# Performance work log

Hardware: AMD Instinct MI355X
Metric: run time of the kernel (lower is better)

Reference implementation:

```python
import jax, jax.numpy as jnp
import numpy as np

EPS = 1e-5  # torch LayerNorm default

def layernorm(x, gamma, beta):
    mu = jnp.mean(x, axis=-1, keepdims=True)
    var = jnp.mean(jnp.square(x - mu), axis=-1, keepdims=True)
    return (x - mu) * jax.lax.rsqrt(var + EPS) * gamma + beta

def setup_inputs() -> dict:
    key = jax.random.key(0)
    ks = jax.random.split(key, 8)
    B, S, D = 4, 2048, 1024
    s = 1.0 / np.sqrt(D)  # torch Linear init scale
    return {
        "x": jax.random.normal(ks[0], (B, S, D), dtype=jnp.float32),
        "Wq": jax.random.uniform(ks[1], (D, D), jnp.float32, -s, s),
        "bq": jax.random.uniform(ks[2], (D,), jnp.float32, -s, s),
        "Wk": jax.random.uniform(ks[3], (D, D), jnp.float32, -s, s),
        "bk": jax.random.uniform(ks[4], (D,), jnp.float32, -s, s),
        "Wv": jax.random.uniform(ks[5], (D, D), jnp.float32, -s, s),
        "bv": jax.random.uniform(ks[6], (D,), jnp.float32, -s, s),
        "gamma": jnp.ones((D,), jnp.float32),
        "beta": jnp.zeros((D,), jnp.float32),
    }

def reference(x, Wq, bq, Wk, bk, Wv, bv, gamma, beta):
    # torch Linear: x @ W.T + b; shared LayerNorm applied to each projection
    q = layernorm(jnp.einsum('bsd,ed->bse', x, Wq) + bq, gamma, beta)
    k = layernorm(jnp.einsum('bsd,ed->bse', x, Wk) + bk, gamma, beta)
    v = layernorm(jnp.einsum('bsd,ed->bse', x, Wv) + bv, gamma, beta)
    att = jnp.einsum('bqd,bkd->bqk', q, k)  # no 1/sqrt(d) scaling in original
    att = jax.nn.softmax(att, axis=-1)
    # dropout is identity in eval mode (reference baseline)
    return jnp.einsum('bqk,bkd->bqd', att, v)
```

## Files before the change

kernel.cpp:

```cpp
#include <hip/hip_runtime.h>

typedef _Float16 f16;
typedef __attribute__((ext_vector_type(4))) _Float16 f16x4;
typedef __attribute__((ext_vector_type(8))) _Float16 f16x8;
typedef __attribute__((ext_vector_type(4))) float f32x4;

#define GLB_AS __attribute__((address_space(1)))
#define LDS_AS __attribute__((address_space(3)))

__device__ __forceinline__ void async_copy16(const void* g, void* l) {
  __builtin_amdgcn_global_load_lds((const GLB_AS void*)g, (LDS_AS void*)l, 16, 0, 0);
}

#define WAITVM(N) asm volatile("s_waitcnt vmcnt(" #N ")" ::: "memory")
#define WAITLGKM0() asm volatile("s_waitcnt lgkmcnt(0)" ::: "memory")
#define BAR() __builtin_amdgcn_s_barrier()
#define SB0() __builtin_amdgcn_sched_barrier(0)

#define STAGE_A(t_, kk_) do {                                                \
    const long _k = (long)(t_) * 64 + (kk_) * 32;                            \
    f16* _d = &Ash[(t_) & 1][kk_][w16 * 32];                                 \
    async_copy16(Ag + _k, _d);                                               \
    if constexpr (IA == 2) async_copy16(Ag + _k + 128l * lda, _d + 4096);    \
  } while (0)
#define STAGE_B(t_, kk_) do {                                                \
    const long _k = (long)(t_) * 64 + (kk_) * 32;                            \
    f16* _d = &Bsh[(t_) & 1][kk_][w16 * 32];                                 \
    async_copy16(Bg + _k, _d);                                               \
    async_copy16(Bg + _k + 128l * ldb, _d + 4096);                           \
  } while (0)

template <int BM, int BN, typename OutT, int MODE, bool BIAS>
__global__ __launch_bounds__(512, 2) void gemm8p(
    const f16* __restrict__ A, const f16* __restrict__ B, OutT* __restrict__ C,
    int lda, int ldb, int ldc, int K, long sA, long sB, long sC,
    int tiles_x, int tiles_y,
    const float* __restrict__ b0, const float* __restrict__ b1,
    const float* __restrict__ b2)
{
  constexpr int WM = BM / 2, WN = BN / 4;
  constexpr int RM = WM / 16, RN = WN / 16;
  constexpr int IA = BM / 128;
  static_assert(RN == 4 && BN == 256, "template assumes BN=256");

  __shared__ __align__(16) f16 Ash[2][2][BM * 32];
  __shared__ __align__(16) f16 Bsh[2][2][BN * 32];

  int bx, by, bz;
  {
    const int n = blockIdx.x;
    if (MODE == 0) {
      by = n % tiles_y;
      const int r = n / tiles_y;
      bx = r % tiles_x;
      bz = r / tiles_x;
    } else {
      const int j = n & 7, i = n >> 3, th = tiles_y >> 1;
      bz = j >> 1;
      bx = i / th;
      by = (j & 1) * th + i % th;
    }
  }

  A += (long)bz * sA;
  B += (long)bz * sB;
  C += (long)bz * sC;

  const int tid  = threadIdx.x;
  const int wave = tid >> 6, lane = tid & 63;
  const int wr = wave >> 2, wc = wave & 3;
  const int m0 = by * BM, n0 = bx * BN;
  const int r16 = lane & 15, quad = lane >> 4;
  const int w16 = wave * 16;

  const int cg8 = (((lane & 3) ^ ((lane >> 2) & 3) ^ ((lane >> 4) & 3)) * 8);
  const f16* Ag = A + (long)(m0 + w16 + (lane >> 2)) * lda + cg8;
  const f16* Bg = B + (long)(n0 + w16 + (lane >> 2)) * ldb + cg8;

  const int NT = K / 64;

  STAGE_A(0, 0); STAGE_B(0, 0);
  STAGE_A(0, 1); STAGE_B(0, 1);
  STAGE_A(1, 0); STAGE_B(1, 0);

  f32x4 acc[RM][RN] = {};

  const int rc  = (quad ^ ((r16 ^ (r16 >> 2)) & 3)) * 8;
  const int rdA = (wr * WM + r16) * 32 + rc;
  const int rdB = (wc * WN + r16) * 32 + rc;

  if constexpr (RM == 8) { WAITVM(8); } else { WAITVM(6); }
  BAR();

  for (int t = 0; t < NT; ++t) {
    const int bp = t & 1;
    const f16* A0 = &Ash[bp][0][0];
    const f16* A1 = &Ash[bp][1][0];
    const f16* B0 = &Bsh[bp][0][0];
    const f16* B1 = &Bsh[bp][1][0];
    f16x8 af[4], bf[4];

    if constexpr (RM == 4) {
#pragma unroll
      for (int i = 0; i < 4; i++) af[i] = *(const f16x8*)&A0[rdA + i * 512];
#pragma unroll
      for (int j = 0; j < 4; j++) bf[j] = *(const f16x8*)&B0[rdB + j * 512];
      if (t + 1 < NT) { STAGE_A(t + 1, 1); STAGE_B(t + 1, 1); }
      BAR();
      WAITLGKM0(); SB0();
      __builtin_amdgcn_s_setprio(1);
#pragma unroll
      for (int i = 0; i < 4; i++)
#pragma unroll
        for (int j = 0; j < 4; j++)
          acc[i][j] = __builtin_amdgcn_mfma_f32_16x16x32_f16(af[i], bf[j], acc[i][j], 0, 0, 0);
      __builtin_amdgcn_s_setprio(0); SB0();
      if (t < NT - 1) { WAITVM(6); } else { WAITVM(0); }
      BAR();
#pragma unroll
      for (int i = 0; i < 4; i++) af[i] = *(const f16x8*)&A1[rdA + i * 512];
#pragma unroll
      for (int j = 0; j < 4; j++) bf[j] = *(const f16x8*)&B1[rdB + j * 512];
      if (t + 2 < NT) { STAGE_A(t + 2, 0); STAGE_B(t + 2, 0); }
      BAR();
      WAITLGKM0(); SB0();
      __builtin_amdgcn_s_setprio(1);
#pragma unroll
      for (int i = 0; i < 4; i++)
#pragma unroll
        for (int j = 0; j < 4; j++)
          acc[i][j] = __builtin_amdgcn_mfma_f32_16x16x32_f16(af[i], bf[j], acc[i][j], 0, 0, 0);
      __builtin_amdgcn_s_setprio(0); SB0();
      if (t < NT - 2) { WAITVM(6); } else if (t == NT - 2) { WAITVM(3); } else { WAITVM(0); }
      BAR();
    } else {
#pragma unroll
      for (int i = 0; i < 4; i++) af[i] = *(const f16x8*)&A0[rdA + i * 512];
#pragma unroll
      for (int j = 0; j < 4; j++) bf[j] = *(const f16x8*)&B0[rdB + j * 512];
      if (t + 1 < NT) STAGE_A(t + 1, 1);
      BAR();
      WAITLGKM0(); SB0();
      __builtin_amdgcn_s_setprio(1);
#pragma unroll
      for (int i = 0; i < 4; i++)
#pragma unroll
        for (int j = 0; j < 4; j++)
          acc[i][j] = __builtin_amdgcn_mfma_f32_16x16x32_f16(af[i], bf[j], acc[i][j], 0, 0, 0);
      __builtin_amdgcn_s_setprio(0); SB0();
      BAR();
#pragma unroll
      for (int i = 0; i < 4; i++) af[i] = *(const f16x8*)&A0[rdA + (4 + i) * 512];
      if (t + 1 < NT) STAGE_B(t + 1, 1);
      BAR();
      WAITLGKM0(); SB0();
      __builtin_amdgcn_s_setprio(1);
#pragma unroll
      for (int i = 0; i < 4; i++)
#pragma unroll
        for (int j = 0; j < 4; j++)
          acc[4 + i][j] = __builtin_amdgcn_mfma_f32_16x16x32_f16(af[i], bf[j], acc[4 + i][j], 0, 0, 0);
      __builtin_amdgcn_s_setprio(0); SB0();
      if (t < NT - 1) { WAITVM(6); } else { WAITVM(0); }
      BAR();
#pragma unroll
      for (int i = 0; i < 4; i++) af[i] = *(const f16x8*)&A1[rdA + i * 512];
#pragma unroll
      for (int j = 0; j < 4; j++) bf[j] = *(const f16x8*)&B1[rdB + j * 512];
      if (t + 2 < NT) STAGE_A(t + 2, 0);
      BAR();
      WAITLGKM0(); SB0();
      __builtin_amdgcn_s_setprio(1);
#pragma unroll
      for (int i = 0; i < 4; i++)
#pragma unroll
        for (int j = 0; j < 4; j++)
          acc[i][j] = __builtin_amdgcn_mfma_f32_16x16x32_f16(af[i], bf[j], acc[i][j], 0, 0, 0);
      __builtin_amdgcn_s_setprio(0); SB0();
      BAR();
#pragma unroll
      for (int i = 0; i < 4; i++) af[i] = *(const f16x8*)&A1[rdA + (4 + i) * 512];
      if (t + 2 < NT) STAGE_B(t + 2, 0);
      BAR();
      WAITLGKM0(); SB0();
      __builtin_amdgcn_s_setprio(1);
#pragma unroll
      for (int i = 0; i < 4; i++)
#pragma unroll
        for (int j = 0; j < 4; j++)
          acc[4 + i][j] = __builtin_amdgcn_mfma_f32_16x16x32_f16(af[i], bf[j], acc[4 + i][j], 0, 0, 0);
      __builtin_amdgcn_s_setprio(0); SB0();
      if (t < NT - 2) { WAITVM(6); } else if (t == NT - 2) { WAITVM(4); } else { WAITVM(0); }
      BAR();
    }
  }

  float bias_j[RN];
#pragma unroll
  for (int j = 0; j < RN; j++) bias_j[j] = 0.f;
  if constexpr (BIAS) {
    const float* bias = (bz == 0) ? b0 : (bz == 1) ? b1 : b2;
#pragma unroll
    for (int j = 0; j < RN; j++) bias_j[j] = bias[n0 + wc * WN + j * 16 + r16];
  }
#pragma unroll
  for (int i = 0; i < RM; i++)
#pragma unroll
    for (int j = 0; j < RN; j++)
#pragma unroll
      for (int r = 0; r < 4; r++) {
        long row = m0 + wr * WM + i * 16 + quad * 4 + r;
        long col = n0 + wc * WN + j * 16 + r16;
        C[row * (long)ldc + col] = (OutT)(acc[i][j][r] + bias_j[j]);
      }
}

__global__ __launch_bounds__(256) void cast_all(
    const float* __restrict__ x, const float* __restrict__ Wq,
    const float* __restrict__ Wk, const float* __restrict__ Wv,
    f16* __restrict__ Xh, f16* __restrict__ Wh)
{
  const long off = (long)blockIdx.x * 1024 + threadIdx.x * 4;
  const float* src;
  f16* dst;
  if (off < 8388608L) {
    src = x + off;
    dst = Xh + off;
  } else {
    const long o = off - 8388608L;
    src = (o < 1048576L) ? Wq + o
        : (o < 2097152L) ? Wk + (o - 1048576L)
                         : Wv + (o - 2097152L);
    dst = Wh + o;
  }
  const float4 v = *(const float4*)src;
  f16x4 h;
  h.x = (f16)v.x; h.y = (f16)v.y; h.z = (f16)v.z; h.w = (f16)v.w;
  *(f16x4*)dst = h;
}

__global__ __launch_bounds__(256) void ln_kernel(
    f16* __restrict__ P, const float* __restrict__ gamma,
    const float* __restrict__ beta)
{
  f16* p = P + (long)blockIdx.y * 8388608 + (long)blockIdx.x * 1024;
  const int tid = threadIdx.x;
  const int e = tid * 4;

  f16x4 raw = *(const f16x4*)(p + e);
  float v0 = (float)raw.x, v1 = (float)raw.y;
  float v2 = (float)raw.z, v3 = (float)raw.w;
  float s  = v0 + v1 + v2 + v3;
  float s2 = v0 * v0 + v1 * v1 + v2 * v2 + v3 * v3;

#pragma unroll
  for (int off = 32; off > 0; off >>= 1) {
    s  += __shfl_down(s, off, 64);
    s2 += __shfl_down(s2, off, 64);
  }
  __shared__ float red[10];
  const int wave = tid >> 6, lane = tid & 63;
  if (lane == 0) { red[wave] = s; red[4 + wave] = s2; }
  __syncthreads();
  if (tid == 0) {
    red[8] = red[0] + red[1] + red[2] + red[3];
    red[9] = red[4] + red[5] + red[6] + red[7];
  }
  __syncthreads();
  const float mu   = red[8] * (1.f / 1024.f);
  const float var  = red[9] * (1.f / 1024.f) - mu * mu;
  const float rstd = rsqrtf(var + 1e-5f);

  float4 gg = *(const float4*)(gamma + e);
  float4 be = *(const float4*)(beta + e);
  f16x4 o;
  o.x = (f16)((v0 - mu) * rstd * gg.x + be.x);
  o.y = (f16)((v1 - mu) * rstd * gg.y + be.y);
  o.z = (f16)((v2 - mu) * rstd * gg.z + be.z);
  o.w = (f16)((v3 - mu) * rstd * gg.w + be.w);
  *(f16x4*)(p + e) = o;
}

__global__ __launch_bounds__(256) void transpose_kernel(const f16* __restrict__ V,
                                                        f16* __restrict__ Vt)
{
  const int S = 2048, D = 1024;
  const f16* v = V + (long)blockIdx.z * ((long)S * D);
  f16* vt = Vt + (long)blockIdx.z * ((long)D * S);
  __shared__ f16 tile[64][66];
  const int d0 = blockIdx.x * 64, j0 = blockIdx.y * 64;
  const int tx = threadIdx.x & 63, ty = threadIdx.x >> 6;
#pragma unroll
  for (int r = ty; r < 64; r += 4)
    tile[r][tx] = v[(long)(j0 + r) * D + d0 + tx];
  __syncthreads();
#pragma unroll
  for (int r = ty; r < 64; r += 4)
    vt[(long)(d0 + r) * S + j0 + tx] = tile[tx][r];
}

__global__ __launch_bounds__(256) void softmax_kernel(float* __restrict__ Sc)
{
  float* srow = Sc + (long)blockIdx.x * 2048;
  const int tid = threadIdx.x;
  float4 a = ((const float4*)srow)[tid];
  float4 b = ((const float4*)srow)[256 + tid];

  float m = fmaxf(fmaxf(fmaxf(a.x, a.y), fmaxf(a.z, a.w)),
                  fmaxf(fmaxf(b.x, b.y), fmaxf(b.z, b.w)));
#pragma unroll
  for (int off = 32; off > 0; off >>= 1) m = fmaxf(m, __shfl_down(m, off, 64));
  __shared__ float red[6];
  const int wave = tid >> 6, lane = tid & 63;
  if (lane == 0) red[wave] = m;
  __syncthreads();
  if (tid == 0) red[4] = fmaxf(fmaxf(red[0], red[1]), fmaxf(red[2], red[3]));
  __syncthreads();
  const float M = red[4];

  a.x = __expf(a.x - M); a.y = __expf(a.y - M);
  a.z = __expf(a.z - M); a.w = __expf(a.w - M);
  b.x = __expf(b.x - M); b.y = __expf(b.y - M);
  b.z = __expf(b.z - M); b.w = __expf(b.w - M);
  float s = a.x + a.y + a.z + a.w + b.x + b.y + b.z + b.w;
#pragma unroll
  for (int off = 32; off > 0; off >>= 1) s += __shfl_down(s, off, 64);
  if (lane == 0) red[wave] = s;
  __syncthreads();
  if (tid == 0) red[5] = red[0] + red[1] + red[2] + red[3];
  __syncthreads();
  const float inv = 1.0f / red[5];

  f16* orow = (f16*)srow;
  f16x4 oa, ob;
  oa.x = (f16)(a.x * inv); oa.y = (f16)(a.y * inv);
  oa.z = (f16)(a.z * inv); oa.w = (f16)(a.w * inv);
  ob.x = (f16)(b.x * inv); ob.y = (f16)(b.y * inv);
  ob.z = (f16)(b.z * inv); ob.w = (f16)(b.w * inv);
  ((f16x4*)orow)[tid]       = oa;
  ((f16x4*)orow)[256 + tid] = ob;
}

extern "C" void kernel_launch(void* const* d_in, const int* in_sizes, int n_in,
                              void* d_out, int out_size, void* d_ws, size_t ws_size,
                              hipStream_t stream)
{
  const float* x     = (const float*)d_in[0];
  const float* Wq    = (const float*)d_in[1];
  const float* bq    = (const float*)d_in[2];
  const float* Wk    = (const float*)d_in[3];
  const float* bk    = (const float*)d_in[4];
  const float* Wv    = (const float*)d_in[5];
  const float* bv    = (const float*)d_in[6];
  const float* gamma = (const float*)d_in[7];
  const float* beta  = (const float*)d_in[8];
  float* out = (float*)d_out;

  char* ws = (char*)d_ws;
  f16*   P  = (f16*)(ws);
  f16*   Vt = (f16*)(ws + (48u << 20));
  float* Sc = (float*)(ws + (64u << 20));
  f16*   Xh = (f16*)(ws + (64u << 20));
  f16*   Wh = (f16*)(ws + (80u << 20));

  cast_all<<<11264, 256, 0, stream>>>(x, Wq, Wk, Wv, Xh, Wh);

  gemm8p<128, 256, f16, 0, true><<<768, 512, 0, stream>>>(
      Xh, Wh, P, 1024, 1024, 1024, 1024, 0L, 1048576L, 8388608L,
      4, 64, bq, bk, bv);

  ln_kernel<<<dim3(8192, 3), 256, 0, stream>>>(P, gamma, beta);

  transpose_kernel<<<dim3(16, 32, 4), 256, 0, stream>>>(P + 2L * 8388608, Vt);

  gemm8p<256, 256, float, 1, false><<<256, 512, 0, stream>>>(
      P, P + 8388608, Sc, 1024, 1024, 2048, 1024, 2097152L, 2097152L, 4194304L,
      8, 8, nullptr, nullptr, nullptr);

  softmax_kernel<<<8192, 256, 0, stream>>>(Sc);

  gemm8p<128, 256, float, 1, false><<<256, 512, 0, stream>>>(
      (const f16*)Sc, Vt, out, 4096, 2048, 1024, 2048, 8388608L, 2097152L, 2097152L,
      4, 16, nullptr, nullptr, nullptr);
}
```

Measured before the change: 300.2 us.

## Replace QKV projection GEMM with simpler 128x128 double-buffered MFMA kernel

Adds a new gemm_kn kernel with 128x128 tiles, BK=32, 256 threads, double-buffered LDS async loads and swizzled LDS reads, and uses it for the fused QKV projection in place of the 8-wave 128x256 pipelined kernel. The smaller tile gives more blocks (1536) and higher occupancy (4 blocks per CU), aiming at better load balance and latency hiding. In exchange it has lower data reuse per tile, a single sync per short K step, and uncoalesced scalar epilogue stores.

Result: no change. 300.7 us (+0.2%).

```diff
diff --git a/kernel.cpp b/kernel.cpp
--- a/kernel.cpp
+++ b/kernel.cpp
@@ -16,6 +16,104 @@
 #define WAITLGKM0() asm volatile("s_waitcnt lgkmcnt(0)" ::: "memory")
 #define BAR() __builtin_amdgcn_s_barrier()
 #define SB0() __builtin_amdgcn_sched_barrier(0)
+
+template <typename OutT, int MODE, bool BIAS>
+__global__ __launch_bounds__(256, 4) void gemm_kn(
+    const f16* __restrict__ A, const f16* __restrict__ B, OutT* __restrict__ C,
+    int lda, int ldb, int ldc, int K, long sA, long sB, long sC,
+    int tiles_x, int tiles_y,
+    const float* __restrict__ b0, const float* __restrict__ b1,
+    const float* __restrict__ b2)
+{
+  constexpr int BM = 128, BK = 32;
+  __shared__ __align__(16) f16 Ash[2][BM * BK];
+  __shared__ __align__(16) f16 Bsh[2][BM * BK];
+
+  int bx, by, bz;
+  {
+    const int n = blockIdx.x;
+    if (MODE == 0) {
+      by = n % tiles_y;
+      const int r = n / tiles_y;
+      bx = r % tiles_x;
+      bz = r / tiles_x;
+    } else {
+      const int j = n & 7, i = n >> 3;
+      bz = j >> 1;
+      bx = i >> 3;
+      by = (j & 1) * 8 + (i & 7);
+    }
+  }
+
+  A += (long)bz * sA;
+  B += (long)bz * sB;
+  C += (long)bz * sC;
+
+  const int tid  = threadIdx.x;
+  const int wave = tid >> 6, lane = tid & 63;
+  const int m0 = by * BM, n0 = bx * BM;
+  const int wm = (wave >> 1) * 64, wn = (wave & 1) * 64;
+  const int r16 = lane & 15, quad = lane >> 4;
+
+  const int srow = wave * 32 + (lane >> 2);
+  const int skb  = ((lane & 3) ^ ((lane >> 3) & 3)) * 8;
+  const f16* Ag = A + (long)(m0 + srow) * lda + skb;
+  const f16* Bg = B + (long)(n0 + srow) * ldb + skb;
+  const int lo0 = (wave * 32) * BK;
+  const int lo1 = (wave * 32 + 16) * BK;
+
+  async_copy16(Ag,                  &Ash[0][lo0]);
+  async_copy16(Ag + 16 * (long)lda, &Ash[0][lo1]);
+  async_copy16(Bg,                  &Bsh[0][lo0]);
+  async_copy16(Bg + 16 * (long)ldb, &Bsh[0][lo1]);
+
+  f32x4 acc[4][4] = {};
+
+  const int cchunk = (quad ^ ((r16 >> 1) & 3)) * 8;
+
+  int buf = 0;
+  for (int k0 = 0; k0 < K; k0 += BK, buf ^= 1) {
+    __syncthreads();
+
+    if (k0 + BK < K) {
+      const int nb = buf ^ 1;
+      const long k1 = k0 + BK;
+      async_copy16(Ag + k1,                  &Ash[nb][lo0]);
+      async_copy16(Ag + k1 + 16 * (long)lda, &Ash[nb][lo1]);
+      async_copy16(Bg + k1,                  &Bsh[nb][lo0]);
+      async_copy16(Bg + k1 + 16 * (long)ldb, &Bsh[nb][lo1]);
+    }
+
+    f16x8 bf[4];
+#pragma unroll
+    for (int j = 0; j < 4; j++)
+      bf[j] = *(const f16x8*)&Bsh[buf][(wn + j * 16 + r16) * BK + cchunk];
+#pragma unroll
+    for (int i = 0; i < 4; i++) {
+      f16x8 af = *(const f16x8*)&Ash[buf][(wm + i * 16 + r16) * BK + cchunk];
+#pragma unroll
+      for (int j = 0; j < 4; j++)
+        acc[i][j] = __builtin_amdgcn_mfma_f32_16x16x32_f16(af, bf[j], acc[i][j], 0, 0, 0);
+    }
+  }
+
+  float bias_j[4] = {0.f, 0.f, 0.f, 0.f};
+  if (BIAS) {
+    const float* bias = (bz == 0) ? b0 : (bz == 1) ? b1 : b2;
+#pragma unroll
+    for (int j = 0; j < 4; j++) bias_j[j] = bias[n0 + wn + j * 16 + r16];
+  }
+#pragma unroll
+  for (int i = 0; i < 4; i++)
+#pragma unroll
+    for (int j = 0; j < 4; j++)
+#pragma unroll
+      for (int r = 0; r < 4; r++) {
+        long row = m0 + wm + i * 16 + quad * 4 + r;
+        long col = n0 + wn + j * 16 + r16;
+        C[row * (long)ldc + col] = (OutT)(acc[i][j][r] + bias_j[j]);
+      }
+}
 
 #define STAGE_A(t_, kk_) do {                                                \
     const long _k = (long)(t_) * 64 + (kk_) * 32;                            \
@@ -365,9 +463,9 @@
 
   cast_all<<<11264, 256, 0, stream>>>(x, Wq, Wk, Wv, Xh, Wh);
 
-  gemm8p<128, 256, f16, 0, true><<<768, 512, 0, stream>>>(
+  gemm_kn<f16, 0, true><<<1536, 256, 0, stream>>>(
       Xh, Wh, P, 1024, 1024, 1024, 1024, 0L, 1048576L, 8388608L,
-      4, 64, bq, bk, bv);
+      8, 64, bq, bk, bv);
 
   ln_kernel<<<dim3(8192, 3), 256, 0, stream>>>(P, gamma, beta);
 
```
